# Kernel tuning notes

Measured on AMD Instinct MI355X. Metric: run time of the kernel, lower is better.

Reference implementation:

```python
import jax, jax.numpy as jnp
from jax import lax
import numpy as np

H, W_DIM = 4096, 4096
KH, KW = 2, 2


def setup_inputs() -> dict:
    key = jax.random.key(0)
    kx, kw = jax.random.split(key)
    X = jax.random.normal(kx, (H, W_DIM), dtype=jnp.float32)
    W = jax.random.uniform(kw, (KH, KW), dtype=jnp.float32)
    return {"X": X, "W": W}


def _conv_valid(X, W):
    # VALID 2D cross-correlation: Y[i,j] = sum_{a,b} X[i+a, j+b] * W[a,b]
    x = X[None, None]          # [1,1,H,W]
    k = W[None, None]          # [1,1,kh,kw]
    y = lax.conv_general_dilated(x, k, window_strides=(1, 1), padding='VALID')
    return y[0, 0]             # [H-kh+1, W-kw+1]


def _trans_conv(X, W):
    # Transposed conv (scatter-add of X[i,j]*W) == full *convolution* with W,
    # i.e. cross-correlation with the spatially flipped kernel, padding kh-1/kw-1.
    x = X[None, None]
    k = W[::-1, ::-1][None, None]
    y = lax.conv_general_dilated(x, k, window_strides=(1, 1),
                                 padding=[(KH - 1, KH - 1), (KW - 1, KW - 1)])
    return y[0, 0]             # back to [H, W]


def reference(X, W):
    y1 = _conv_valid(X, W)     # [H-1, W-1]
    y2 = _trans_conv(y1, W)    # [H, W]
    return y2
```

## Files before the change

kernel.cpp:

```cpp
#include <hip/hip_runtime.h>


#define HD 4096
#define QPR 1024
#define RB 8

typedef float f32x4 __attribute__((ext_vector_type(4)));

__global__ __launch_bounds__(256) void fused_conv_kernel(
    const float* __restrict__ X, const float* __restrict__ Wk,
    float* __restrict__ Y)
{
    const int idx  = blockIdx.x * blockDim.x + threadIdx.x;
    const int i0   = (idx >> 10) * RB;
    const int j0   = (idx & (QPR - 1)) << 2;
    const int lane = threadIdx.x & 63;

    const float w00 = Wk[0], w01 = Wk[1], w10 = Wk[2], w11 = Wk[3];

    float x[RB + 2][6];
    #pragma unroll
    for (int r = 0; r < RB + 2; ++r) {
        const int row = i0 - 1 + r;
        if (row >= 0 && row < HD) {
            const float* rp = X + (size_t)row * HD;
            const f32x4 v = *reinterpret_cast<const f32x4*>(rp + j0);
            float lft = __shfl_up(v[3], 1);
            float rgt = __shfl_down(v[0], 1);
            const int  eoff = (lane == 0) ? (j0 - 1) : (j0 + 4);
            const bool need = ((lane == 0) || (lane == 63)) &&
                              (eoff >= 0) && (eoff < HD);
            const float ev  = need ? rp[eoff] : 0.f;
            if (lane == 0)  lft = ev;
            if (lane == 63) rgt = ev;
            x[r][0] = lft;  x[r][1] = v[0]; x[r][2] = v[1];
            x[r][3] = v[2]; x[r][4] = v[3]; x[r][5] = rgt;
        } else {
            #pragma unroll
            for (int c = 0; c < 6; ++c) x[r][c] = 0.f;
        }
    }

    const bool lv = (j0 > 0);
    const bool rv = (j0 + 4 < HD);

    float y1p[5], y1c[5];
    {
        const bool pv = (i0 > 0);
        #pragma unroll
        for (int q = 0; q < 5; ++q) {
            const float v = w00 * x[0][q] + w01 * x[0][q + 1]
                          + w10 * x[1][q] + w11 * x[1][q + 1];
            const bool ok = pv && (q != 0 || lv) && (q != 4 || rv);
            y1p[q] = ok ? v : 0.f;
        }
    }

    #pragma unroll
    for (int r = 0; r < RB; ++r) {
        const int i = i0 + r;
        const bool pv = (i < HD - 1);
        #pragma unroll
        for (int q = 0; q < 5; ++q) {
            const float v = w00 * x[r + 1][q] + w01 * x[r + 1][q + 1]
                          + w10 * x[r + 2][q] + w11 * x[r + 2][q + 1];
            const bool ok = pv && (q != 0 || lv) && (q != 4 || rv);
            y1c[q] = ok ? v : 0.f;
        }

        f32x4 o;
        o[0] = w00 * y1c[1] + w01 * y1c[0] + w10 * y1p[1] + w11 * y1p[0];
        o[1] = w00 * y1c[2] + w01 * y1c[1] + w10 * y1p[2] + w11 * y1p[1];
        o[2] = w00 * y1c[3] + w01 * y1c[2] + w10 * y1p[3] + w11 * y1p[2];
        o[3] = w00 * y1c[4] + w01 * y1c[3] + w10 * y1p[4] + w11 * y1p[3];
        __builtin_nontemporal_store(o, reinterpret_cast<f32x4*>(Y + (size_t)i * HD + j0));

        #pragma unroll
        for (int q = 0; q < 5; ++q) y1p[q] = y1c[q];
    }
}

extern "C" void kernel_launch(void* const* d_in, const int* in_sizes, int n_in,
                              void* d_out, int out_size, void* d_ws, size_t ws_size,
                              hipStream_t stream) {
    const float* X  = (const float*)d_in[0];
    const float* Wk = (const float*)d_in[1];
    float* Y        = (float*)d_out;

    const int total_threads = (HD / RB) * QPR;
    const int block = 256;
    const int grid  = total_threads / block;
    fused_conv_kernel<<<grid, block, 0, stream>>>(X, Wk, Y);
}
```

Before: 116.1 us.

## Stream input rows with prefetch and add a boundary-free interior path

Replaces loading all RB+2 input rows up front with a rolling three-row window that prefetches the next row while computing the current output row. Adds a templated interior specialization that skips the row and column bounds checks and masking for tiles away from the image edges. This lowers register pressure and branch overhead, but it also reduces the number of loads in flight per thread at once, which could hurt latency hiding in this memory-bound kernel.

```diff
diff --git a/kernel.cpp b/kernel.cpp
--- a/kernel.cpp
+++ b/kernel.cpp
@@ -2,10 +2,101 @@
 
 
 #define HD 4096
-#define QPR 1024
 #define RB 8
 
 typedef float f32x4 __attribute__((ext_vector_type(4)));
+
+template<bool INT>
+__device__ __forceinline__ void load_row(const float* __restrict__ X, int row,
+                                         int j0, int lane, f32x4& v, float& ev)
+{
+    ev = 0.f;
+    if (INT || (unsigned)row < (unsigned)HD) {
+        const float* rp = X + (size_t)row * HD;
+        v = *reinterpret_cast<const f32x4*>(rp + j0);
+        const int eoff = (lane == 0) ? (j0 - 1) : (j0 + 4);
+        bool need = (lane == 0) || (lane == 63);
+        if (!INT) need = need && (eoff >= 0) && (eoff < HD);
+        if (need) ev = rp[eoff];
+    } else {
+        v[0] = 0.f; v[1] = 0.f; v[2] = 0.f; v[3] = 0.f;
+    }
+}
+
+__device__ __forceinline__ void make_x(const f32x4 v, const float ev, int lane,
+                                       float x[6])
+{
+    float lft = __shfl_up(v[3], 1);
+    float rgt = __shfl_down(v[0], 1);
+    if (lane == 0)  lft = ev;
+    if (lane == 63) rgt = ev;
+    x[0] = lft; x[1] = v[0]; x[2] = v[1]; x[3] = v[2]; x[4] = v[3]; x[5] = rgt;
+}
+
+template<bool INT>
+__device__ __forceinline__ void y1_row(const float xa[6], const float xb[6],
+                                       float w00, float w01, float w10, float w11,
+                                       bool pv, bool lv, bool rv, float y[5])
+{
+    #pragma unroll
+    for (int q = 0; q < 5; ++q) {
+        float v = w00 * xa[q] + w01 * xa[q + 1]
+                + w10 * xb[q] + w11 * xb[q + 1];
+        if (!INT) {
+            const bool ok = pv && (q != 0 || lv) && (q != 4 || rv);
+            v = ok ? v : 0.f;
+        }
+        y[q] = v;
+    }
+}
+
+template<bool INT>
+__device__ __forceinline__ void tile(const float* __restrict__ X,
+                                     float* __restrict__ Y,
+                                     int i0, int j0, int lane,
+                                     float w00, float w01, float w10, float w11)
+{
+    const bool lv = INT || (j0 > 0);
+    const bool rv = INT || (j0 + 4 < HD);
+
+    f32x4 v0, vnxt; float e0, enxt;
+    load_row<INT>(X, i0 - 1, j0, lane, v0, e0);
+    f32x4 vcur; float ecur;
+    load_row<INT>(X, i0,     j0, lane, vcur, ecur);
+    load_row<INT>(X, i0 + 1, j0, lane, vnxt, enxt);
+
+    float xa[6], xb[6], xc[6];
+    make_x(v0, e0, lane, xa);
+    make_x(vcur, ecur, lane, xb);
+
+    float y1p[5], y1c[5];
+    y1_row<INT>(xa, xb, w00, w01, w10, w11, (i0 > 0), lv, rv, y1p);
+
+    #pragma unroll
+    for (int r = 0; r < RB; ++r) {
+        const int i = i0 + r;
+        f32x4 vpf; float epf;
+        if (r < RB - 1)
+            load_row<INT>(X, i + 2, j0, lane, vpf, epf);
+
+        make_x(vnxt, enxt, lane, xc);
+        y1_row<INT>(xb, xc, w00, w01, w10, w11, (i < HD - 1), lv, rv, y1c);
+
+        f32x4 o;
+        o[0] = w00 * y1c[1] + w01 * y1c[0] + w10 * y1p[1] + w11 * y1p[0];
+        o[1] = w00 * y1c[2] + w01 * y1c[1] + w10 * y1p[2] + w11 * y1p[1];
+        o[2] = w00 * y1c[3] + w01 * y1c[2] + w10 * y1p[3] + w11 * y1p[2];
+        o[3] = w00 * y1c[4] + w01 * y1c[3] + w10 * y1p[4] + w11 * y1p[3];
+        __builtin_nontemporal_store(o,
+            reinterpret_cast<f32x4*>(Y + (size_t)i * HD + j0));
+
+        #pragma unroll
+        for (int q = 0; q < 5; ++q) y1p[q] = y1c[q];
+        #pragma unroll
+        for (int c = 0; c < 6; ++c) xb[c] = xc[c];
+        if (r < RB - 1) { vnxt = vpf; enxt = epf; }
+    }
+}
 
 __global__ __launch_bounds__(256) void fused_conv_kernel(
     const float* __restrict__ X, const float* __restrict__ Wk,
@@ -13,71 +104,17 @@
 {
     const int idx  = blockIdx.x * blockDim.x + threadIdx.x;
     const int i0   = (idx >> 10) * RB;
-    const int j0   = (idx & (QPR - 1)) << 2;
+    const int j0   = (idx & 1023) << 2;
     const int lane = threadIdx.x & 63;
 
     const float w00 = Wk[0], w01 = Wk[1], w10 = Wk[2], w11 = Wk[3];
 
-    float x[RB + 2][6];
-    #pragma unroll
-    for (int r = 0; r < RB + 2; ++r) {
-        const int row = i0 - 1 + r;
-        if (row >= 0 && row < HD) {
-            const float* rp = X + (size_t)row * HD;
-            const f32x4 v = *reinterpret_cast<const f32x4*>(rp + j0);
-            float lft = __shfl_up(v[3], 1);
-            float rgt = __shfl_down(v[0], 1);
-            const int  eoff = (lane == 0) ? (j0 - 1) : (j0 + 4);
-            const bool need = ((lane == 0) || (lane == 63)) &&
-                              (eoff >= 0) && (eoff < HD);
-            const float ev  = need ? rp[eoff] : 0.f;
-            if (lane == 0)  lft = ev;
-            if (lane == 63) rgt = ev;
-            x[r][0] = lft;  x[r][1] = v[0]; x[r][2] = v[1];
-            x[r][3] = v[2]; x[r][4] = v[3]; x[r][5] = rgt;
-        } else {
-            #pragma unroll
-            for (int c = 0; c < 6; ++c) x[r][c] = 0.f;
-        }
-    }
+    const int jw0 = ((idx & 1023) - lane) << 2;
+    const bool interior = (i0 >= RB) && (i0 <= HD - 2 * RB) &&
+                          (jw0 != 0) && (jw0 != HD - 256);
 
-    const bool lv = (j0 > 0);
-    const bool rv = (j0 + 4 < HD);
-
-    float y1p[5], y1c[5];
-    {
-        const bool pv = (i0 > 0);
-        #pragma unroll
-        for (int q = 0; q < 5; ++q) {
-            const float v = w00 * x[0][q] + w01 * x[0][q + 1]
-                          + w10 * x[1][q] + w11 * x[1][q + 1];
-            const bool ok = pv && (q != 0 || lv) && (q != 4 || rv);
-            y1p[q] = ok ? v : 0.f;
-        }
-    }
-
-    #pragma unroll
-    for (int r = 0; r < RB; ++r) {
-        const int i = i0 + r;
-        const bool pv = (i < HD - 1);
-        #pragma unroll
-        for (int q = 0; q < 5; ++q) {
-            const float v = w00 * x[r + 1][q] + w01 * x[r + 1][q + 1]
-                          + w10 * x[r + 2][q] + w11 * x[r + 2][q + 1];
-            const bool ok = pv && (q != 0 || lv) && (q != 4 || rv);
-            y1c[q] = ok ? v : 0.f;
-        }
-
-        f32x4 o;
-        o[0] = w00 * y1c[1] + w01 * y1c[0] + w10 * y1p[1] + w11 * y1p[0];
-        o[1] = w00 * y1c[2] + w01 * y1c[1] + w10 * y1p[2] + w11 * y1p[1];
-        o[2] = w00 * y1c[3] + w01 * y1c[2] + w10 * y1p[3] + w11 * y1p[2];
-        o[3] = w00 * y1c[4] + w01 * y1c[3] + w10 * y1p[4] + w11 * y1p[3];
-        __builtin_nontemporal_store(o, reinterpret_cast<f32x4*>(Y + (size_t)i * HD + j0));
-
-        #pragma unroll
-        for (int q = 0; q < 5; ++q) y1p[q] = y1c[q];
-    }
+    if (interior) tile<true >(X, Y, i0, j0, lane, w00, w01, w10, w11);
+    else          tile<false>(X, Y, i0, j0, lane, w00, w01, w10, w11);
 }
 
 extern "C" void kernel_launch(void* const* d_in, const int* in_sizes, int n_in,
@@ -87,7 +124,7 @@
     const float* Wk = (const float*)d_in[1];
     float* Y        = (float*)d_out;
 
-    const int total_threads = (HD / RB) * QPR;
+    const int total_threads = (HD / RB) * (HD / 4);
     const int block = 256;
     const int grid  = total_threads / block;
     fused_conv_kernel<<<grid, block, 0, stream>>>(X, Wk, Y);
```

Result: faster. 113.4 us (-2.3%).
